# Performance work log

Measured on AMD Instinct MI355X. Metric: run time of the kernel, lower is better.

## Reference

```python
import jax, jax.numpy as jnp
import numpy as np

B, X_DIM, Y_DIM, HIDDEN = 512, 768, 128, 1024
H2 = HIDDEN // 2


def setup_inputs() -> dict:
    key = jax.random.key(0)
    ks = jax.random.split(key, 10)
    s_in = 1.0 / np.sqrt(X_DIM)
    s_h = 1.0 / np.sqrt(H2)
    return {
        "x_samples": jax.random.normal(ks[0], (B, X_DIM), jnp.float32),
        "y_samples": jax.random.normal(ks[1], (B, Y_DIM), jnp.float32),
        "w1_mu": jax.random.uniform(ks[2], (X_DIM, H2), jnp.float32, -s_in, s_in),
        "b1_mu": jax.random.uniform(ks[3], (H2,), jnp.float32, -s_in, s_in),
        "w2_mu": jax.random.uniform(ks[4], (H2, Y_DIM), jnp.float32, -s_h, s_h),
        "b2_mu": jax.random.uniform(ks[5], (Y_DIM,), jnp.float32, -s_h, s_h),
        "w1_lv": jax.random.uniform(ks[6], (X_DIM, H2), jnp.float32, -s_in, s_in),
        "b1_lv": jax.random.uniform(ks[7], (H2,), jnp.float32, -s_in, s_in),
        "w2_lv": jax.random.uniform(ks[8], (H2, Y_DIM), jnp.float32, -s_h, s_h),
        "b2_lv": jax.random.uniform(ks[9], (Y_DIM,), jnp.float32, -s_h, s_h),
    }


def reference(x_samples, y_samples, w1_mu, b1_mu, w2_mu, b2_mu,
              w1_lv, b1_lv, w2_lv, b2_lv):
    batch = y_samples.shape[0]
    # p_mu / p_logvar MLP heads
    mu = jax.nn.relu(x_samples @ w1_mu + b1_mu) @ w2_mu + b2_mu          # [B, Y]
    logvar = jnp.tanh(jax.nn.relu(x_samples @ w1_lv + b1_lv) @ w2_lv + b2_lv)  # [B, Y]

    inv_var = jnp.exp(-logvar)
    # positive: diagonal Gaussian log-prob of y_i under p(.|x_i), up to const
    positive = (-0.5 * (mu - y_samples) ** 2 * inv_var - 0.5 * logvar).sum(-1)  # [B]

    # pairwise log-probs: row i = params from x_i, col j = sample y_j
    mu_1 = mu[:, None, :]            # [B, 1, Y]
    lv_1 = logvar[:, None, :]        # [B, 1, Y]
    y_1 = y_samples[None, :, :]      # [1, B, Y]
    all_probs = (-0.5 * (y_1 - mu_1) ** 2 * jnp.exp(-lv_1) - 0.5 * lv_1).sum(-1)  # [B, B]

    # Faithful replication of the torch broadcasting: diag_mask is [B, B, 1],
    # so all_probs + diag_mask broadcasts to [B, B, B], then logsumexp over dim 0.
    diag_mask = (jnp.eye(batch, dtype=all_probs.dtype) * -20.0)[:, :, None]  # [B, B, 1]
    logits = all_probs + diag_mask                                           # [B, B, B]
    negative = jax.scipy.special.logsumexp(logits, axis=0) - jnp.log(batch - 1.0)  # [B, B]

    return (positive - negative).mean()
```

## Files before the change

### kernel.cpp

```cpp
#include <hip/hip_runtime.h>
#include <math.h>

#define BSZ   512
#define XD    768
#define YD    128
#define H2D   512

__global__ __launch_bounds__(256, 2) void layer1_kernel(
    const float* __restrict__ x,
    const float* __restrict__ w1_mu, const float* __restrict__ w1_lv,
    float* __restrict__ p1)
{
    __shared__ float As[16][132];
    __shared__ float Bs[16][68];

    const int t      = threadIdx.x;
    const int branch = blockIdx.z >> 3;
    const int ks     = blockIdx.z & 7;
    const float* __restrict__ W = branch ? w1_lv : w1_mu;
    float* __restrict__ out = p1 + (size_t)blockIdx.z * (BSZ * H2D);

    const int m0 = blockIdx.x * 128;
    const int n0 = blockIdx.y * 64;
    const int tx = t & 15;
    const int ty = t >> 4;

    const int am  = t >> 1;
    const int akq = (t & 1) * 8;
    const int bkk = t >> 4;
    const int bnq = (t & 15) * 4;

    const int kbase = ks * 96;
    float acc[8][4] = {};

    float4 a0p = *(const float4*)&x[(m0 + am) * XD + kbase + akq];
    float4 a1p = *(const float4*)&x[(m0 + am) * XD + kbase + akq + 4];
    float4 bp  = *(const float4*)&W[(kbase + bkk) * H2D + n0 + bnq];

    for (int kt = 0; kt < 96; kt += 16) {
        __syncthreads();
        As[akq + 0][am] = a0p.x; As[akq + 1][am] = a0p.y;
        As[akq + 2][am] = a0p.z; As[akq + 3][am] = a0p.w;
        As[akq + 4][am] = a1p.x; As[akq + 5][am] = a1p.y;
        As[akq + 6][am] = a1p.z; As[akq + 7][am] = a1p.w;
        *(float4*)&Bs[bkk][bnq] = bp;
        __syncthreads();
        if (kt + 16 < 96) {
            const int kn = kbase + kt + 16;
            a0p = *(const float4*)&x[(m0 + am) * XD + kn + akq];
            a1p = *(const float4*)&x[(m0 + am) * XD + kn + akq + 4];
            bp  = *(const float4*)&W[(kn + bkk) * H2D + n0 + bnq];
        }
        #pragma unroll
        for (int k = 0; k < 16; ++k) {
            const float4 a0 = *(const float4*)&As[k][ty * 8];
            const float4 a1 = *(const float4*)&As[k][ty * 8 + 4];
            const float4 bv = *(const float4*)&Bs[k][tx * 4];
            acc[0][0] += a0.x*bv.x; acc[0][1] += a0.x*bv.y; acc[0][2] += a0.x*bv.z; acc[0][3] += a0.x*bv.w;
            acc[1][0] += a0.y*bv.x; acc[1][1] += a0.y*bv.y; acc[1][2] += a0.y*bv.z; acc[1][3] += a0.y*bv.w;
            acc[2][0] += a0.z*bv.x; acc[2][1] += a0.z*bv.y; acc[2][2] += a0.z*bv.z; acc[2][3] += a0.z*bv.w;
            acc[3][0] += a0.w*bv.x; acc[3][1] += a0.w*bv.y; acc[3][2] += a0.w*bv.z; acc[3][3] += a0.w*bv.w;
            acc[4][0] += a1.x*bv.x; acc[4][1] += a1.x*bv.y; acc[4][2] += a1.x*bv.z; acc[4][3] += a1.x*bv.w;
            acc[5][0] += a1.y*bv.x; acc[5][1] += a1.y*bv.y; acc[5][2] += a1.y*bv.z; acc[5][3] += a1.y*bv.w;
            acc[6][0] += a1.z*bv.x; acc[6][1] += a1.z*bv.y; acc[6][2] += a1.z*bv.z; acc[6][3] += a1.z*bv.w;
            acc[7][0] += a1.w*bv.x; acc[7][1] += a1.w*bv.y; acc[7][2] += a1.w*bv.z; acc[7][3] += a1.w*bv.w;
        }
    }

    #pragma unroll
    for (int i = 0; i < 8; ++i) {
        const float4 o = make_float4(acc[i][0], acc[i][1], acc[i][2], acc[i][3]);
        *(float4*)&out[(m0 + ty * 8 + i) * H2D + n0 + tx * 4] = o;
    }
}

__global__ __launch_bounds__(256, 2) void layer2_kernel(
    const float* __restrict__ p1,
    const float* __restrict__ b1_mu, const float* __restrict__ b1_lv,
    const float* __restrict__ w2_mu, const float* __restrict__ w2_lv,
    const float* __restrict__ y,
    float* __restrict__ p2,
    double* __restrict__ Sy, double* __restrict__ Sy2,
    double* __restrict__ accum, unsigned int* __restrict__ counter)
{
    __shared__ float As[16][36];
    __shared__ float Bs[16][132];
    const int t = threadIdx.x;

    if (blockIdx.z == 32) {
        const int id = blockIdx.x;
        const int dl = t & 7;
        const int g  = t >> 3;
        const int d  = id * 8 + dl;
        float s = 0.f, s2 = 0.f;
        #pragma unroll
        for (int i = g * 16; i < g * 16 + 16; ++i) {
            const float v = y[i * YD + d];
            s += v; s2 += v * v;
        }
        float* shs  = &As[0][0];
        float* shs2 = &Bs[0][0];
        shs[t] = s; shs2[t] = s2;
        __syncthreads();
        if (t < 8) {
            double S = 0.0, S2 = 0.0;
            #pragma unroll
            for (int gg = 0; gg < 32; ++gg) {
                S += (double)shs[gg * 8 + t]; S2 += (double)shs2[gg * 8 + t];
            }
            Sy[id * 8 + t] = S; Sy2[id * 8 + t] = S2;
        } else if (id == 0 && t == 8)  { accum[0] = 0.0; }
        else if (id == 0 && t == 9)  { accum[1] = 0.0; }
        else if (id == 0 && t == 10) { *counter = 0u; }
        return;
    }

    const int branch = blockIdx.z >> 4;
    const int ks2    = blockIdx.z & 15;
    const float* __restrict__ q  = p1 + (size_t)(branch * 8) * (BSZ * H2D);
    const float* __restrict__ b1 = branch ? b1_lv : b1_mu;
    const float* __restrict__ W  = branch ? w2_lv : w2_mu;
    float* __restrict__ out = p2 + (size_t)blockIdx.z * (BSZ * YD);

    const int m0 = blockIdx.x * 32;
    const int tx = t & 15;
    const int ty = t >> 4;

    const int am  = t >> 2;
    const int akq = (t & 3) * 4;
    const int bkk = t >> 4;
    const int bnq = (t & 15) * 8;

    const int kbase = ks2 * 32;
    float acc[2][2][4] = {};

    float4 aval, bb4;
    if (t < 128) {
        const int arow = (m0 + am) * H2D + kbase + akq;
        aval = *(const float4*)&q[arow];
        #pragma unroll
        for (int s = 1; s < 8; ++s) {
            const float4 v = *(const float4*)&q[(size_t)s * (BSZ * H2D) + arow];
            aval.x += v.x; aval.y += v.y; aval.z += v.z; aval.w += v.w;
        }
        bb4 = *(const float4*)&b1[kbase + akq];
    }
    float4 w0 = *(const float4*)&W[(kbase + bkk) * YD + bnq];
    float4 w1 = *(const float4*)&W[(kbase + bkk) * YD + bnq + 4];

    for (int kt = 0; kt < 32; kt += 16) {
        __syncthreads();
        if (t < 128) {
            As[akq + 0][am] = fmaxf(aval.x + bb4.x, 0.f);
            As[akq + 1][am] = fmaxf(aval.y + bb4.y, 0.f);
            As[akq + 2][am] = fmaxf(aval.z + bb4.z, 0.f);
            As[akq + 3][am] = fmaxf(aval.w + bb4.w, 0.f);
        }
        *(float4*)&Bs[bkk][bnq]     = w0;
        *(float4*)&Bs[bkk][bnq + 4] = w1;
        __syncthreads();
        if (kt == 0) {
            const int kn = kbase + 16;
            if (t < 128) {
                const int arow = (m0 + am) * H2D + kn + akq;
                aval = *(const float4*)&q[arow];
                #pragma unroll
                for (int s = 1; s < 8; ++s) {
                    const float4 v = *(const float4*)&q[(size_t)s * (BSZ * H2D) + arow];
                    aval.x += v.x; aval.y += v.y; aval.z += v.z; aval.w += v.w;
                }
                bb4 = *(const float4*)&b1[kn + akq];
            }
            w0 = *(const float4*)&W[(kn + bkk) * YD + bnq];
            w1 = *(const float4*)&W[(kn + bkk) * YD + bnq + 4];
        }
        #pragma unroll
        for (int k = 0; k < 16; ++k) {
            const float a0 = As[k][ty * 2 + 0];
            const float a1 = As[k][ty * 2 + 1];
            const float4 v0 = *(const float4*)&Bs[k][tx * 4];
            const float4 v1 = *(const float4*)&Bs[k][64 + tx * 4];
            acc[0][0][0] += a0*v0.x; acc[0][0][1] += a0*v0.y; acc[0][0][2] += a0*v0.z; acc[0][0][3] += a0*v0.w;
            acc[0][1][0] += a0*v1.x; acc[0][1][1] += a0*v1.y; acc[0][1][2] += a0*v1.z; acc[0][1][3] += a0*v1.w;
            acc[1][0][0] += a1*v0.x; acc[1][0][1] += a1*v0.y; acc[1][0][2] += a1*v0.z; acc[1][0][3] += a1*v0.w;
            acc[1][1][0] += a1*v1.x; acc[1][1][1] += a1*v1.y; acc[1][1][2] += a1*v1.z; acc[1][1][3] += a1*v1.w;
        }
    }

    #pragma unroll
    for (int r = 0; r < 2; ++r) {
        const int row = (m0 + ty * 2 + r) * YD;
        float4 o0 = make_float4(acc[r][0][0], acc[r][0][1], acc[r][0][2], acc[r][0][3]);
        float4 o1 = make_float4(acc[r][1][0], acc[r][1][1], acc[r][1][2], acc[r][1][3]);
        *(float4*)&out[row + tx * 4]      = o0;
        *(float4*)&out[row + 64 + tx * 4] = o1;
    }
}

__global__ __launch_bounds__(256) void reduce_kernel(
    const float* __restrict__ p2, const float* __restrict__ y,
    const float* __restrict__ b2_mu, const float* __restrict__ b2_lv,
    const double* __restrict__ Sy, const double* __restrict__ Sy2,
    double* __restrict__ accum, unsigned int* __restrict__ counter,
    float* __restrict__ outp)
{
    const int NE = BSZ * YD;
    const int e  = blockIdx.x * 256 + threadIdx.x;
    const int d  = e & (YD - 1);

    float mu = b2_mu[d];
    float lp = b2_lv[d];
    #pragma unroll
    for (int s = 0; s < 16; ++s) {
        mu += p2[s * NE + e];
        lp += p2[(16 + s) * NE + e];
    }
    const float lv = tanhf(lp);
    const float iv = expf(-lv);
    const float dm = mu - y[e];

    double pos = -0.5 * (double)dm * (double)dm * (double)iv - 0.5 * (double)lv;
    double ap  = (double)iv * (-0.5 * Sy2[d] + (double)mu * Sy[d]
                               - 256.0 * (double)mu * (double)mu)
               - 256.0 * (double)lv;

    #pragma unroll
    for (int off = 32; off > 0; off >>= 1) {
        pos += __shfl_down(pos, off);
        ap  += __shfl_down(ap, off);
    }
    __shared__ double sp[4];
    __shared__ double sa[4];
    const int lane = threadIdx.x & 63;
    const int wv   = threadIdx.x >> 6;
    if (lane == 0) { sp[wv] = pos; sa[wv] = ap; }
    __syncthreads();
    if (threadIdx.x == 0) {
        atomicAdd(&accum[0], sp[0] + sp[1] + sp[2] + sp[3]);
        atomicAdd(&accum[1], sa[0] + sa[1] + sa[2] + sa[3]);
        __threadfence();
        const unsigned int old = atomicAdd(counter, 1u);
        if (old == 255u) {
            const double P = atomicAdd(&accum[0], 0.0);
            const double A = atomicAdd(&accum[1], 0.0);
            const double C = log1p(exp(-20.0) / 511.0);
            outp[0] = (float)(P / 512.0 - A / 262144.0 - C);
        }
    }
}

extern "C" void kernel_launch(void* const* d_in, const int* in_sizes, int n_in,
                              void* d_out, int out_size, void* d_ws, size_t ws_size,
                              hipStream_t stream) {
    const float* x     = (const float*)d_in[0];
    const float* y     = (const float*)d_in[1];
    const float* w1_mu = (const float*)d_in[2];
    const float* b1_mu = (const float*)d_in[3];
    const float* w2_mu = (const float*)d_in[4];
    const float* b2_mu = (const float*)d_in[5];
    const float* w1_lv = (const float*)d_in[6];
    const float* b1_lv = (const float*)d_in[7];
    const float* w2_lv = (const float*)d_in[8];
    const float* b2_lv = (const float*)d_in[9];

    char* ws = (char*)d_ws;
    float*  p1 = (float*)(ws);
    float*  p2 = (float*)(ws + (size_t)16 * BSZ * H2D * 4);
    double* Sy = (double*)(ws + (size_t)16 * BSZ * H2D * 4
                              + (size_t)32 * BSZ * YD * 4);
    double* Sy2 = Sy + YD;
    double* accum = Sy2 + YD;
    unsigned int* counter = (unsigned int*)(accum + 2);

    layer1_kernel<<<dim3(4, 8, 16), 256, 0, stream>>>(x, w1_mu, w1_lv, p1);
    layer2_kernel<<<dim3(16, 1, 33), 256, 0, stream>>>(
        p1, b1_mu, b1_lv, w2_mu, w2_lv, y, p2, Sy, Sy2, accum, counter);
    reduce_kernel<<<256, 256, 0, stream>>>(
        p2, y, b2_mu, b2_lv, Sy, Sy2, accum, counter, (float*)d_out);
}
```

Before: 112.3 us.

## Enlarge layer1 tiles with 16-way split-K and register-resident W2 in layer2

Layer1 now uses 128x128 output tiles with 8x8 per-thread micro-tiles and splits K into 16 slices of 48 instead of 8 of 96, keeping the block count at 512 while raising FMA-to-shared-load ratio. Layer2 is rewritten to sum 16 split-K partials plus bias and ReLU into a single shared tile, then has each lane hold its W2 column slice in registers and compute 8 rows per wave. The cost is twice as many layer1 partial buffers written and read back, more workspace, and higher register pressure from the 64 accumulators and 64 W2 registers.

```diff
diff --git a/kernel.cpp b/kernel.cpp
--- a/kernel.cpp
+++ b/kernel.cpp
@@ -12,65 +12,69 @@
     float* __restrict__ p1)
 {
     __shared__ float As[16][132];
-    __shared__ float Bs[16][68];
+    __shared__ float Bs[16][132];
 
     const int t      = threadIdx.x;
-    const int branch = blockIdx.z >> 3;
-    const int ks     = blockIdx.z & 7;
+    const int branch = blockIdx.z >> 4;
+    const int ks     = blockIdx.z & 15;
     const float* __restrict__ W = branch ? w1_lv : w1_mu;
     float* __restrict__ out = p1 + (size_t)blockIdx.z * (BSZ * H2D);
 
     const int m0 = blockIdx.x * 128;
-    const int n0 = blockIdx.y * 64;
+    const int n0 = blockIdx.y * 128;
     const int tx = t & 15;
     const int ty = t >> 4;
 
     const int am  = t >> 1;
     const int akq = (t & 1) * 8;
     const int bkk = t >> 4;
-    const int bnq = (t & 15) * 4;
-
-    const int kbase = ks * 96;
-    float acc[8][4] = {};
+    const int bnq = (t & 15) * 8;
+
+    const int kbase = ks * 48;
+    float acc[8][8] = {};
 
     float4 a0p = *(const float4*)&x[(m0 + am) * XD + kbase + akq];
     float4 a1p = *(const float4*)&x[(m0 + am) * XD + kbase + akq + 4];
-    float4 bp  = *(const float4*)&W[(kbase + bkk) * H2D + n0 + bnq];
-
-    for (int kt = 0; kt < 96; kt += 16) {
+    float4 b0p = *(const float4*)&W[(kbase + bkk) * H2D + n0 + bnq];
+    float4 b1p = *(const float4*)&W[(kbase + bkk) * H2D + n0 + bnq + 4];
+
+    for (int kt = 0; kt < 48; kt += 16) {
         __syncthreads();
         As[akq + 0][am] = a0p.x; As[akq + 1][am] = a0p.y;
         As[akq + 2][am] = a0p.z; As[akq + 3][am] = a0p.w;
         As[akq + 4][am] = a1p.x; As[akq + 5][am] = a1p.y;
         As[akq + 6][am] = a1p.z; As[akq + 7][am] = a1p.w;
-        *(float4*)&Bs[bkk][bnq] = bp;
+        *(float4*)&Bs[bkk][bnq]     = b0p;
+        *(float4*)&Bs[bkk][bnq + 4] = b1p;
         __syncthreads();
-        if (kt + 16 < 96) {
+        if (kt + 16 < 48) {
             const int kn = kbase + kt + 16;
             a0p = *(const float4*)&x[(m0 + am) * XD + kn + akq];
             a1p = *(const float4*)&x[(m0 + am) * XD + kn + akq + 4];
-            bp  = *(const float4*)&W[(kn + bkk) * H2D + n0 + bnq];
+            b0p = *(const float4*)&W[(kn + bkk) * H2D + n0 + bnq];
+            b1p = *(const float4*)&W[(kn + bkk) * H2D + n0 + bnq + 4];
         }
         #pragma unroll
         for (int k = 0; k < 16; ++k) {
             const float4 a0 = *(const float4*)&As[k][ty * 8];
             const float4 a1 = *(const float4*)&As[k][ty * 8 + 4];
-            const float4 bv = *(const float4*)&Bs[k][tx * 4];
-            acc[0][0] += a0.x*bv.x; acc[0][1] += a0.x*bv.y; acc[0][2] += a0.x*bv.z; acc[0][3] += a0.x*bv.w;
-            acc[1][0] += a0.y*bv.x; acc[1][1] += a0.y*bv.y; acc[1][2] += a0.y*bv.z; acc[1][3] += a0.y*bv.w;
-            acc[2][0] += a0.z*bv.x; acc[2][1] += a0.z*bv.y; acc[2][2] += a0.z*bv.z; acc[2][3] += a0.z*bv.w;
-            acc[3][0] += a0.w*bv.x; acc[3][1] += a0.w*bv.y; acc[3][2] += a0.w*bv.z; acc[3][3] += a0.w*bv.w;
-            acc[4][0] += a1.x*bv.x; acc[4][1] += a1.x*bv.y; acc[4][2] += a1.x*bv.z; acc[4][3] += a1.x*bv.w;
-            acc[5][0] += a1.y*bv.x; acc[5][1] += a1.y*bv.y; acc[5][2] += a1.y*bv.z; acc[5][3] += a1.y*bv.w;
-            acc[6][0] += a1.z*bv.x; acc[6][1] += a1.z*bv.y; acc[6][2] += a1.z*bv.z; acc[6][3] += a1.z*bv.w;
-            acc[7][0] += a1.w*bv.x; acc[7][1] += a1.w*bv.y; acc[7][2] += a1.w*bv.z; acc[7][3] += a1.w*bv.w;
+            const float4 b0 = *(const float4*)&Bs[k][tx * 8];
+            const float4 b1 = *(const float4*)&Bs[k][tx * 8 + 4];
+            const float av[8] = {a0.x, a0.y, a0.z, a0.w, a1.x, a1.y, a1.z, a1.w};
+            const float bv[8] = {b0.x, b0.y, b0.z, b0.w, b1.x, b1.y, b1.z, b1.w};
+            #pragma unroll
+            for (int i = 0; i < 8; ++i)
+                #pragma unroll
+                for (int j = 0; j < 8; ++j)
+                    acc[i][j] += av[i] * bv[j];
         }
     }
 
     #pragma unroll
     for (int i = 0; i < 8; ++i) {
-        const float4 o = make_float4(acc[i][0], acc[i][1], acc[i][2], acc[i][3]);
-        *(float4*)&out[(m0 + ty * 8 + i) * H2D + n0 + tx * 4] = o;
+        const int row = (m0 + ty * 8 + i) * H2D + n0 + tx * 8;
+        *(float4*)&out[row]     = make_float4(acc[i][0], acc[i][1], acc[i][2], acc[i][3]);
+        *(float4*)&out[row + 4] = make_float4(acc[i][4], acc[i][5], acc[i][6], acc[i][7]);
     }
 }
 
@@ -83,8 +87,7 @@
     double* __restrict__ Sy, double* __restrict__ Sy2,
     double* __restrict__ accum, unsigned int* __restrict__ counter)
 {
-    __shared__ float As[16][36];
-    __shared__ float Bs[16][132];
+    __shared__ float Hc[32][36];
     const int t = threadIdx.x;
 
     if (blockIdx.z == 32) {
@@ -98,8 +101,8 @@
             const float v = y[i * YD + d];
             s += v; s2 += v * v;
         }
-        float* shs  = &As[0][0];
-        float* shs2 = &Bs[0][0];
+        float* shs  = &Hc[0][0];
+        float* shs2 = &Hc[0][0] + 512;
         shs[t] = s; shs2[t] = s2;
         __syncthreads();
         if (t < 8) {
@@ -117,83 +120,59 @@
 
     const int branch = blockIdx.z >> 4;
     const int ks2    = blockIdx.z & 15;
-    const float* __restrict__ q  = p1 + (size_t)(branch * 8) * (BSZ * H2D);
+    const float* __restrict__ q  = p1 + (size_t)(branch * 16) * (BSZ * H2D);
     const float* __restrict__ b1 = branch ? b1_lv : b1_mu;
     const float* __restrict__ W  = branch ? w2_lv : w2_mu;
     float* __restrict__ out = p2 + (size_t)blockIdx.z * (BSZ * YD);
 
-    const int m0 = blockIdx.x * 32;
-    const int tx = t & 15;
-    const int ty = t >> 4;
-
-    const int am  = t >> 2;
-    const int akq = (t & 3) * 4;
-    const int bkk = t >> 4;
-    const int bnq = (t & 15) * 8;
-
-    const int kbase = ks2 * 32;
-    float acc[2][2][4] = {};
-
-    float4 aval, bb4;
-    if (t < 128) {
-        const int arow = (m0 + am) * H2D + kbase + akq;
-        aval = *(const float4*)&q[arow];
-        #pragma unroll
-        for (int s = 1; s < 8; ++s) {
-            const float4 v = *(const float4*)&q[(size_t)s * (BSZ * H2D) + arow];
-            aval.x += v.x; aval.y += v.y; aval.z += v.z; aval.w += v.w;
-        }
-        bb4 = *(const float4*)&b1[kbase + akq];
-    }
-    float4 w0 = *(const float4*)&W[(kbase + bkk) * YD + bnq];
-    float4 w1 = *(const float4*)&W[(kbase + bkk) * YD + bnq + 4];
-
-    for (int kt = 0; kt < 32; kt += 16) {
-        __syncthreads();
-        if (t < 128) {
-            As[akq + 0][am] = fmaxf(aval.x + bb4.x, 0.f);
-            As[akq + 1][am] = fmaxf(aval.y + bb4.y, 0.f);
-            As[akq + 2][am] = fmaxf(aval.z + bb4.z, 0.f);
-            As[akq + 3][am] = fmaxf(aval.w + bb4.w, 0.f);
-        }
-        *(float4*)&Bs[bkk][bnq]     = w0;
-        *(float4*)&Bs[bkk][bnq + 4] = w1;
-        __syncthreads();
-        if (kt == 0) {
-            const int kn = kbase + 16;
-            if (t < 128) {
-                const int arow = (m0 + am) * H2D + kn + akq;
-                aval = *(const float4*)&q[arow];
-                #pragma unroll
-                for (int s = 1; s < 8; ++s) {
-                    const float4 v = *(const float4*)&q[(size_t)s * (BSZ * H2D) + arow];
-                    aval.x += v.x; aval.y += v.y; aval.z += v.z; aval.w += v.w;
-                }
-                bb4 = *(const float4*)&b1[kn + akq];
-            }
-            w0 = *(const float4*)&W[(kn + bkk) * YD + bnq];
-            w1 = *(const float4*)&W[(kn + bkk) * YD + bnq + 4];
-        }
-        #pragma unroll
-        for (int k = 0; k < 16; ++k) {
-            const float a0 = As[k][ty * 2 + 0];
-            const float a1 = As[k][ty * 2 + 1];
-            const float4 v0 = *(const float4*)&Bs[k][tx * 4];
-            const float4 v1 = *(const float4*)&Bs[k][64 + tx * 4];
-            acc[0][0][0] += a0*v0.x; acc[0][0][1] += a0*v0.y; acc[0][0][2] += a0*v0.z; acc[0][0][3] += a0*v0.w;
-            acc[0][1][0] += a0*v1.x; acc[0][1][1] += a0*v1.y; acc[0][1][2] += a0*v1.z; acc[0][1][3] += a0*v1.w;
-            acc[1][0][0] += a1*v0.x; acc[1][0][1] += a1*v0.y; acc[1][0][2] += a1*v0.z; acc[1][0][3] += a1*v0.w;
-            acc[1][1][0] += a1*v1.x; acc[1][1][1] += a1*v1.y; acc[1][1][2] += a1*v1.z; acc[1][1][3] += a1*v1.w;
-        }
-    }
-
-    #pragma unroll
-    for (int r = 0; r < 2; ++r) {
-        const int row = (m0 + ty * 2 + r) * YD;
-        float4 o0 = make_float4(acc[r][0][0], acc[r][0][1], acc[r][0][2], acc[r][0][3]);
-        float4 o1 = make_float4(acc[r][1][0], acc[r][1][1], acc[r][1][2], acc[r][1][3]);
-        *(float4*)&out[row + tx * 4]      = o0;
-        *(float4*)&out[row + 64 + tx * 4] = o1;
+    const int m0   = blockIdx.x * 32;
+    const int kb   = ks2 * 32;
+    const int lane = t & 63;
+    const int wave = t >> 6;
+
+    float br0[32], br1[32];
+    #pragma unroll
+    for (int k = 0; k < 32; ++k) {
+        br0[k] = W[(kb + k) * YD + lane];
+        br1[k] = W[(kb + k) * YD + 64 + lane];
+    }
+
+    {
+        const int row = t >> 3;
+        const int kq  = (t & 7) * 4;
+        const int base = (m0 + row) * H2D + kb + kq;
+        float4 h = *(const float4*)&b1[kb + kq];
+        #pragma unroll
+        for (int s = 0; s < 16; ++s) {
+            const float4 v = *(const float4*)&q[(size_t)s * (BSZ * H2D) + base];
+            h.x += v.x; h.y += v.y; h.z += v.z; h.w += v.w;
+        }
+        h.x = fmaxf(h.x, 0.f); h.y = fmaxf(h.y, 0.f);
+        h.z = fmaxf(h.z, 0.f); h.w = fmaxf(h.w, 0.f);
+        *(float4*)&Hc[row][kq] = h;
+    }
+    __syncthreads();
+
+    const int wm0 = wave * 8;
+    float acc0[8] = {}, acc1[8] = {};
+    #pragma unroll
+    for (int m = 0; m < 8; ++m) {
+        const float* hrow = &Hc[wm0 + m][0];
+        #pragma unroll
+        for (int qd = 0; qd < 8; ++qd) {
+            const float4 a4 = *(const float4*)&hrow[qd * 4];
+            acc0[m] += a4.x * br0[qd * 4 + 0]; acc1[m] += a4.x * br1[qd * 4 + 0];
+            acc0[m] += a4.y * br0[qd * 4 + 1]; acc1[m] += a4.y * br1[qd * 4 + 1];
+            acc0[m] += a4.z * br0[qd * 4 + 2]; acc1[m] += a4.z * br1[qd * 4 + 2];
+            acc0[m] += a4.w * br0[qd * 4 + 3]; acc1[m] += a4.w * br1[qd * 4 + 3];
+        }
+    }
+
+    #pragma unroll
+    for (int m = 0; m < 8; ++m) {
+        const int row = (m0 + wm0 + m) * YD;
+        out[row + lane]      = acc0[m];
+        out[row + 64 + lane] = acc1[m];
     }
 }
 
@@ -265,14 +244,14 @@
 
     char* ws = (char*)d_ws;
     float*  p1 = (float*)(ws);
-    float*  p2 = (float*)(ws + (size_t)16 * BSZ * H2D * 4);
-    double* Sy = (double*)(ws + (size_t)16 * BSZ * H2D * 4
+    float*  p2 = (float*)(ws + (size_t)32 * BSZ * H2D * 4);
+    double* Sy = (double*)(ws + (size_t)32 * BSZ * H2D * 4
                               + (size_t)32 * BSZ * YD * 4);
     double* Sy2 = Sy + YD;
     double* accum = Sy2 + YD;
     unsigned int* counter = (unsigned int*)(accum + 2);
 
-    layer1_kernel<<<dim3(4, 8, 16), 256, 0, stream>>>(x, w1_mu, w1_lv, p1);
+    layer1_kernel<<<dim3(4, 4, 32), 256, 0, stream>>>(x, w1_mu, w1_lv, p1);
     layer2_kernel<<<dim3(16, 1, 33), 256, 0, stream>>>(
         p1, b1_mu, b1_lv, w2_mu, w2_lv, y, p2, Sy, Sy2, accum, counter);
     reduce_kernel<<<256, 256, 0, stream>>>(
```

New measurement: 121.6 us. 1.08x slower.
